# Kernel tuning notes

Measured on AMD Instinct MI355X. Metric: run time of the kernel, lower is better.

Reference implementation:

```python
import jax, jax.numpy as jnp
import numpy as np

N_GROUPS = 8
TOPK_GROUPS = 4
TOPK = 8
ROUTE_SCALE = 2.5

def setup_inputs() -> dict:
    key = jax.random.key(0)
    k1, k2, k3 = jax.random.split(key, 3)
    B, D, E = 8192, 7168, 256
    x = jax.random.normal(k1, (B, D), dtype=jnp.float32)
    weight = jax.random.normal(k2, (E, D), dtype=jnp.float32) / np.sqrt(D)
    bias = jax.random.normal(k3, (E,), dtype=jnp.float32) * 0.01
    return {"x": x, "weight": weight, "bias": bias}

def reference(x, weight, bias):
    B = x.shape[0]
    # linear scores: (B, E)
    scores = jnp.einsum('bd,ed->be', x, weight)
    # sigmoid score function
    s = jax.nn.sigmoid(scores)
    original_scores = s
    # bias correction for group selection (bias is not None since dim==7168)
    sb = s + bias
    # group view: (B, G, E/G)
    sg = sb.reshape(B, N_GROUPS, -1)
    # group score = sum of top-2 per group (bias branch)
    group_scores = jax.lax.top_k(sg, 2)[0].sum(axis=-1)  # (B, G)
    gidx = jax.lax.top_k(group_scores, TOPK_GROUPS)[1]   # (B, topk_groups)
    # boolean mask of selected groups
    gmask = jnp.zeros((B, N_GROUPS), dtype=bool).at[jnp.arange(B)[:, None], gidx].set(True)
    sg = jnp.where(gmask[:, :, None], sg, -jnp.inf)
    flat = sg.reshape(B, -1)  # (B, E)
    indices = jax.lax.top_k(flat, TOPK)[1]               # (B, topk)
    weights = jnp.take_along_axis(original_scores, indices, axis=1)
    # sigmoid path: normalize to sum 1, then scale
    weights = weights / weights.sum(axis=-1, keepdims=True)
    weights = weights * ROUTE_SCALE
    return weights.astype(x.dtype), indices
```

## Files before the change

### kernel.cpp

```cpp
#include <hip/hip_runtime.h>
#include <hip/hip_bf16.h>
#include <math.h>

#define DDIM 7168
#define NEXP 256
#define NGRP 8
#define TOPKG 4
#define TOPK 8
#define ROUTE_SCALE 2.5f

#define BM 64
#define BN 256
#define BK 32
#define KSPLIT 4
#define KPER (DDIM / KSPLIT)
#define NSTEP (KPER / BK)
#define NKTILE (DDIM / BK)
#define BT_ELEMS (NEXP * BK * 2)

typedef __attribute__((ext_vector_type(8))) short bf16x8;
typedef __attribute__((ext_vector_type(4))) float f32x4;
typedef unsigned int u32;
typedef unsigned short ushort_t;

static __device__ __forceinline__ ushort_t bf16_rne(float f) {
    u32 b = __float_as_uint(f);
    u32 r = (b + 0x7fffu + ((b >> 16) & 1u)) >> 16;
    return (ushort_t)r;
}
static __device__ __forceinline__ float bf16_to_f32(ushort_t h) {
    return __uint_as_float(((u32)h) << 16);
}
static __device__ __forceinline__ void split_elem(float f, short& h, short& l) {
    union { __hip_bfloat16 b; short s; } cv;
    cv.b = __float2bfloat16(f);
    h = cv.s;
    float hf = __uint_as_float(((u32)(ushort_t)cv.s) << 16);
    cv.b = __float2bfloat16(f - hf);
    l = cv.s;
}

__global__ __launch_bounds__(256) void wsplit_kernel(const float* __restrict__ w,
                                                     short* __restrict__ wsp)
{
    const int kt = blockIdx.x;
    const int e  = threadIdx.x;
    const float* wp = w + (size_t)e * DDIM + (size_t)kt * BK;
    short* tb = wsp + (size_t)kt * BT_ELEMS;
    const int fn = e >> 4, er = e & 15;
    #pragma unroll
    for (int jg = 0; jg < 4; jg++) {
        float f[8];
        *(float4*)&f[0] = *(const float4*)(wp + jg * 8);
        *(float4*)&f[4] = *(const float4*)(wp + jg * 8 + 4);
        ushort_t h[8], l[8];
        #pragma unroll
        for (int j = 0; j < 8; j++) {
            h[j] = bf16_rne(f[j]);
            l[j] = bf16_rne(f[j] - bf16_to_f32(h[j]));
        }
        const int lane = jg * 16 + er;
        *(uint4*)(tb + ((size_t)(0 * 16 + fn) * 64 + lane) * 8) = *(uint4*)h;
        *(uint4*)(tb + ((size_t)(1 * 16 + fn) * 64 + lane) * 8) = *(uint4*)l;
    }
}

__global__ __launch_bounds__(512, 2) void gemm_split_kernel(
    const float* __restrict__ x, const short* __restrict__ wsp,
    float* __restrict__ part, int Btok)
{
    __shared__ short Blds[2][BT_ELEMS];
    __shared__ float Alds[2][BM * BK];

    const int bid  = blockIdx.x;
    const int xcd  = bid & 7;
    const int ksp  = xcd & 3;
    const int mt   = (bid >> 3) * 2 + (xcd >> 2);
    const int m0   = mt * BM;
    const int kbase = ksp * KPER;
    const int t    = threadIdx.x;
    const int wid  = t >> 6, lane = t & 63;
    const int wm   = wid >> 2, wn = wid & 3;
    const int lr   = lane & 15, lg = lane >> 4;

    const short* wt0 = wsp + (size_t)(ksp * NSTEP) * BT_ELEMS;

    const int arow  = wid * 8 + (lane >> 3);
    const int akoff = 4 * ((lane & 7) ^ ((lane >> 3) & 7));
    const float* asrc0 = x + (size_t)(m0 + arow) * DDIM + kbase + akoff;
    const int adst_off = wid * 1024 + lane * 16;

#define STAGE_B(stp, buf) do {                                                             \
        const short* gt_ = wt0 + (size_t)(stp) * BT_ELEMS;                                 \
        _Pragma("unroll")                                                                  \
        for (int i_ = 0; i_ < 4; i_++) {                                                   \
            const int off_ = wid * 4096 + i_ * 1024;                                       \
            __builtin_amdgcn_global_load_lds(                                              \
                (const __attribute__((address_space(1))) u32*)((const char*)gt_ + off_ + lane * 16), \
                (__attribute__((address_space(3))) u32*)((char*)&Blds[buf][0] + off_),     \
                16, 0, 0);                                                                 \
        } } while (0)

#define STAGE_A(stp, buf) do {                                                             \
        __builtin_amdgcn_global_load_lds(                                                  \
            (const __attribute__((address_space(1))) u32*)(asrc0 + (size_t)(stp) * BK),    \
            (__attribute__((address_space(3))) u32*)((char*)&Alds[buf][0] + adst_off),     \
            16, 0, 0);                                                                     \
    } while (0)

    f32x4 acc[2][4];
    #pragma unroll
    for (int i = 0; i < 2; i++)
        #pragma unroll
        for (int j = 0; j < 4; j++) acc[i][j] = (f32x4){0.f, 0.f, 0.f, 0.f};

    STAGE_B(0, 0);
    STAGE_A(0, 0);

    for (int st = 0; st < NSTEP; st++) {
        const int cur = st & 1;
        __syncthreads();

        if (st + 1 < NSTEP) {
            STAGE_B(st + 1, cur ^ 1);
            STAGE_A(st + 1, cur ^ 1);
        }

        const char* ab = (const char*)&Alds[cur][0];
        bf16x8 ah[2], al[2];
        #pragma unroll
        for (int fm = 0; fm < 2; fm++) {
            const int row = wm * 32 + fm * 16 + lr;
            const int rb  = row * 128;
            const int sw  = (lr & 7) << 4;
            float fr[8];
            *(float4*)&fr[0] = *(const float4*)(ab + rb + ((lg * 32) ^ sw));
            *(float4*)&fr[4] = *(const float4*)(ab + rb + ((lg * 32 + 16) ^ sw));
            union { bf16x8 v; short s[8]; } H, L;
            #pragma unroll
            for (int j = 0; j < 8; j++)
                split_elem(fr[j], H.s[j], L.s[j]);
            ah[fm] = H.v;
            al[fm] = L.v;
        }

        bf16x8 bhv[4], blv[4];
        #pragma unroll
        for (int fn = 0; fn < 4; fn++) {
            bhv[fn] = *(const bf16x8*)&Blds[cur][((size_t)(0 * 16 + wn * 4 + fn) * 64 + lane) * 8];
            blv[fn] = *(const bf16x8*)&Blds[cur][((size_t)(1 * 16 + wn * 4 + fn) * 64 + lane) * 8];
        }
        #pragma unroll
        for (int fn = 0; fn < 4; fn++)
            #pragma unroll
            for (int fm = 0; fm < 2; fm++)
                acc[fm][fn] = __builtin_amdgcn_mfma_f32_16x16x32_bf16(ah[fm], bhv[fn], acc[fm][fn], 0, 0, 0);
        #pragma unroll
        for (int fn = 0; fn < 4; fn++)
            #pragma unroll
            for (int fm = 0; fm < 2; fm++)
                acc[fm][fn] = __builtin_amdgcn_mfma_f32_16x16x32_bf16(ah[fm], blv[fn], acc[fm][fn], 0, 0, 0);
        #pragma unroll
        for (int fn = 0; fn < 4; fn++)
            #pragma unroll
            for (int fm = 0; fm < 2; fm++)
                acc[fm][fn] = __builtin_amdgcn_mfma_f32_16x16x32_bf16(al[fm], bhv[fn], acc[fm][fn], 0, 0, 0);
    }
#undef STAGE_B
#undef STAGE_A

    float* pp = part + (size_t)ksp * (size_t)Btok * NEXP;
    #pragma unroll
    for (int fm = 0; fm < 2; fm++) {
        const int row0 = m0 + wm * 32 + fm * 16 + lg * 4;
        #pragma unroll
        for (int fn = 0; fn < 4; fn++) {
            const int col = wn * 64 + fn * 16 + lr;
            #pragma unroll
            for (int rr = 0; rr < 4; rr++)
                pp[(size_t)(row0 + rr) * NEXP + col] = acc[fm][fn][rr];
        }
    }
}

__global__ __launch_bounds__(256) void gate_kernel(
    const float* __restrict__ part, const float* __restrict__ bias,
    float* __restrict__ out_w, float* __restrict__ out_i, int B)
{
    const int lane = threadIdx.x & 63;
    const int wid  = threadIdx.x >> 6;
    const int row  = blockIdx.x * 4 + wid;
    if (row >= B) return;

    const size_t plane = (size_t)B * NEXP;
    const float* pr = part + (size_t)row * NEXP + lane * 4;
    float4 v0 = *(const float4*)(pr);
    float4 v1 = *(const float4*)(pr + plane);
    float4 v2 = *(const float4*)(pr + 2 * plane);
    float4 v3 = *(const float4*)(pr + 3 * plane);
    float sc[4] = { v0.x + v1.x + v2.x + v3.x,
                    v0.y + v1.y + v2.y + v3.y,
                    v0.z + v1.z + v2.z + v3.z,
                    v0.w + v1.w + v2.w + v3.w };
    float4 bv = *(const float4*)(bias + lane * 4);
    const float bb[4] = { bv.x, bv.y, bv.z, bv.w };

    float so[4], sb[4];
    #pragma unroll
    for (int j = 0; j < 4; j++) {
        so[j] = 1.0f / (1.0f + expf(-sc[j]));
        sb[j] = so[j] + bb[j];
    }

    float m1 = sb[0], m2 = -INFINITY;
    #pragma unroll
    for (int j = 1; j < 4; j++) {
        if (sb[j] > m1)      { m2 = m1; m1 = sb[j]; }
        else if (sb[j] > m2) { m2 = sb[j]; }
    }
    #pragma unroll
    for (int m = 1; m <= 4; m <<= 1) {
        float o1 = __shfl_xor(m1, m);
        float o2 = __shfl_xor(m2, m);
        float hi = fmaxf(m1, o1);
        float lo = fminf(m1, o1);
        m1 = hi;
        m2 = fmaxf(lo, fmaxf(m2, o2));
    }
    float gscore = m1 + m2;
    int g = lane >> 3;

    float gs[NGRP];
    #pragma unroll
    for (int gg = 0; gg < NGRP; gg++) gs[gg] = __shfl(gscore, gg * 8);
    int rank = 0;
    #pragma unroll
    for (int gg = 0; gg < NGRP; gg++) {
        if (gg == g) continue;
        if (gs[gg] > gs[g] || (gs[gg] == gs[g] && gg < g)) rank++;
    }
    const bool selg = (rank < TOPKG);
    float mv[4];
    #pragma unroll
    for (int j = 0; j < 4; j++) mv[j] = selg ? sb[j] : -INFINITY;

    float wsel[TOPK];
    int   isel[TOPK];
    float wsum = 0.f;
    #pragma unroll
    for (int it = 0; it < TOPK; it++) {
        float v = mv[0]; int jj = 0;
        #pragma unroll
        for (int j = 1; j < 4; j++)
            if (mv[j] > v) { v = mv[j]; jj = j; }
        int gi = (lane << 2) | jj;
        #pragma unroll
        for (int m = 1; m < 64; m <<= 1) {
            float ov = __shfl_xor(v, m);
            int   oi = __shfl_xor(gi, m);
            if (ov > v || (ov == v && oi < gi)) { v = ov; gi = oi; }
        }
        int slot = gi & 3, src = gi >> 2;
        float cand = (slot == 0) ? so[0] : (slot == 1) ? so[1] : (slot == 2) ? so[2] : so[3];
        float sval = __shfl(cand, src);
        wsel[it] = sval; isel[it] = gi; wsum += sval;
        if (lane == src) mv[slot] = -INFINITY;
    }

    if (lane == 0) {
        float scl = ROUTE_SCALE / wsum;
        #pragma unroll
        for (int it = 0; it < TOPK; it++) {
            out_w[(size_t)row * TOPK + it] = wsel[it] * scl;
            out_i[(size_t)row * TOPK + it] = (float)isel[it];
        }
    }
}

extern "C" void kernel_launch(void* const* d_in, const int* in_sizes, int n_in,
                              void* d_out, int out_size, void* d_ws, size_t ws_size,
                              hipStream_t stream)
{
    const float* x    = (const float*)d_in[0];
    const float* w    = (const float*)d_in[1];
    const float* bias = (const float*)d_in[2];
    const int B = in_sizes[0] / DDIM;

    float* part = (float*)d_ws;
    short* wsp  = (short*)((char*)d_ws + (size_t)KSPLIT * B * NEXP * sizeof(float));

    float* out_w = (float*)d_out;
    float* out_i = out_w + (size_t)B * TOPK;

    hipLaunchKernelGGL(wsplit_kernel, dim3(NKTILE), dim3(256), 0, stream, w, wsp);
    hipLaunchKernelGGL(gemm_split_kernel, dim3((B / BM) * KSPLIT), dim3(512), 0, stream,
                       x, wsp, part, B);
    hipLaunchKernelGGL(gate_kernel, dim3((B + 3) / 4), dim3(256), 0, stream,
                       part, bias, out_w, out_i, B);
}
```

Before: 126.3 us.

## Double the M tile to 128 and triple-buffer LDS staging with explicit waitcnts

Doubles the per-block M tile so each staged weight tile (hi/lo bf16 split) feeds four 16-row fragments instead of two. This halves how often the weight slab is re-read per token row. The LDS pipeline goes from double to triple buffering with rotating pointers and manual s_waitcnt vmcnt/lgkmcnt plus a raw barrier, so two stages are in flight at once. In exchange, LDS use and accumulator registers roughly double, which may cut occupancy below the declared two blocks per CU. The manual wait counts must also exactly match the loads issued per stage.

```diff
diff --git a/kernel.cpp b/kernel.cpp
--- a/kernel.cpp
+++ b/kernel.cpp
@@ -9,7 +9,7 @@
 #define TOPK 8
 #define ROUTE_SCALE 2.5f
 
-#define BM 64
+#define BM 128
 #define BN 256
 #define BK 32
 #define KSPLIT 4
@@ -17,6 +17,7 @@
 #define NSTEP (KPER / BK)
 #define NKTILE (DDIM / BK)
 #define BT_ELEMS (NEXP * BK * 2)
+#define AT_FLOATS (BM * BK)
 
 typedef __attribute__((ext_vector_type(8))) short bf16x8;
 typedef __attribute__((ext_vector_type(4))) float f32x4;
@@ -69,8 +70,8 @@
     const float* __restrict__ x, const short* __restrict__ wsp,
     float* __restrict__ part, int Btok)
 {
-    __shared__ short Blds[2][BT_ELEMS];
-    __shared__ float Alds[2][BM * BK];
+    __shared__ short Blds[3][BT_ELEMS];
+    __shared__ float Alds[3][AT_FLOATS];
 
     const int bid  = blockIdx.x;
     const int xcd  = bid & 7;
@@ -85,52 +86,58 @@
 
     const short* wt0 = wsp + (size_t)(ksp * NSTEP) * BT_ELEMS;
 
-    const int arow  = wid * 8 + (lane >> 3);
+    const int arow0 = wid * 16 + (lane >> 3);
     const int akoff = 4 * ((lane & 7) ^ ((lane >> 3) & 7));
-    const float* asrc0 = x + (size_t)(m0 + arow) * DDIM + kbase + akoff;
-    const int adst_off = wid * 1024 + lane * 16;
-
-#define STAGE_B(stp, buf) do {                                                             \
+    const float* asrc0 = x + (size_t)(m0 + arow0) * DDIM + kbase + akoff;
+    const size_t arow_step = (size_t)8 * DDIM;
+    const int adst0 = wid * 2048 + lane * 16;
+
+#define STAGE_B(stp, bptr) do {                                                            \
         const short* gt_ = wt0 + (size_t)(stp) * BT_ELEMS;                                 \
         _Pragma("unroll")                                                                  \
         for (int i_ = 0; i_ < 4; i_++) {                                                   \
             const int off_ = wid * 4096 + i_ * 1024;                                       \
             __builtin_amdgcn_global_load_lds(                                              \
                 (const __attribute__((address_space(1))) u32*)((const char*)gt_ + off_ + lane * 16), \
-                (__attribute__((address_space(3))) u32*)((char*)&Blds[buf][0] + off_),     \
+                (__attribute__((address_space(3))) u32*)((char*)(bptr) + off_),            \
                 16, 0, 0);                                                                 \
         } } while (0)
 
-#define STAGE_A(stp, buf) do {                                                             \
-        __builtin_amdgcn_global_load_lds(                                                  \
-            (const __attribute__((address_space(1))) u32*)(asrc0 + (size_t)(stp) * BK),    \
-            (__attribute__((address_space(3))) u32*)((char*)&Alds[buf][0] + adst_off),     \
-            16, 0, 0);                                                                     \
-    } while (0)
-
-    f32x4 acc[2][4];
-    #pragma unroll
-    for (int i = 0; i < 2; i++)
+#define STAGE_A(stp, aptr) do {                                                            \
+        _Pragma("unroll")                                                                  \
+        for (int i_ = 0; i_ < 2; i_++) {                                                   \
+            __builtin_amdgcn_global_load_lds(                                              \
+                (const __attribute__((address_space(1))) u32*)(asrc0 + (size_t)i_ * arow_step + (size_t)(stp) * BK), \
+                (__attribute__((address_space(3))) u32*)((char*)(aptr) + adst0 + i_ * 1024), \
+                16, 0, 0);                                                                 \
+        } } while (0)
+
+    f32x4 acc[4][4];
+    #pragma unroll
+    for (int i = 0; i < 4; i++)
         #pragma unroll
         for (int j = 0; j < 4; j++) acc[i][j] = (f32x4){0.f, 0.f, 0.f, 0.f};
 
-    STAGE_B(0, 0);
-    STAGE_A(0, 0);
+    short* pB_r = &Blds[0][0]; short* pB_1 = &Blds[1][0]; short* pB_2 = &Blds[2][0];
+    float* pA_r = &Alds[0][0]; float* pA_1 = &Alds[1][0]; float* pA_2 = &Alds[2][0];
+
+    STAGE_B(0, pB_r); STAGE_A(0, pA_r);
+    STAGE_B(1, pB_1); STAGE_A(1, pA_1);
 
     for (int st = 0; st < NSTEP; st++) {
-        const int cur = st & 1;
-        __syncthreads();
-
-        if (st + 1 < NSTEP) {
-            STAGE_B(st + 1, cur ^ 1);
-            STAGE_A(st + 1, cur ^ 1);
-        }
-
-        const char* ab = (const char*)&Alds[cur][0];
-        bf16x8 ah[2], al[2];
-        #pragma unroll
-        for (int fm = 0; fm < 2; fm++) {
-            const int row = wm * 32 + fm * 16 + lr;
+        if (st < NSTEP - 1) { asm volatile("s_waitcnt vmcnt(6)" ::: "memory"); }
+        else                { asm volatile("s_waitcnt vmcnt(0)" ::: "memory"); }
+        asm volatile("s_waitcnt lgkmcnt(0)" ::: "memory");
+        __builtin_amdgcn_s_barrier();
+        asm volatile("" ::: "memory");
+
+        if (st + 2 < NSTEP) { STAGE_B(st + 2, pB_2); STAGE_A(st + 2, pA_2); }
+
+        const char* ab = (const char*)pA_r;
+        bf16x8 ah[4], al[4];
+        #pragma unroll
+        for (int fm = 0; fm < 4; fm++) {
+            const int row = wm * 64 + fm * 16 + lr;
             const int rb  = row * 128;
             const int sw  = (lr & 7) << 4;
             float fr[8];
@@ -147,32 +154,35 @@
         bf16x8 bhv[4], blv[4];
         #pragma unroll
         for (int fn = 0; fn < 4; fn++) {
-            bhv[fn] = *(const bf16x8*)&Blds[cur][((size_t)(0 * 16 + wn * 4 + fn) * 64 + lane) * 8];
-            blv[fn] = *(const bf16x8*)&Blds[cur][((size_t)(1 * 16 + wn * 4 + fn) * 64 + lane) * 8];
+            bhv[fn] = *(const bf16x8*)&pB_r[((size_t)(0 * 16 + wn * 4 + fn) * 64 + lane) * 8];
+            blv[fn] = *(const bf16x8*)&pB_r[((size_t)(1 * 16 + wn * 4 + fn) * 64 + lane) * 8];
         }
         #pragma unroll
         for (int fn = 0; fn < 4; fn++)
             #pragma unroll
-            for (int fm = 0; fm < 2; fm++)
+            for (int fm = 0; fm < 4; fm++)
                 acc[fm][fn] = __builtin_amdgcn_mfma_f32_16x16x32_bf16(ah[fm], bhv[fn], acc[fm][fn], 0, 0, 0);
         #pragma unroll
         for (int fn = 0; fn < 4; fn++)
             #pragma unroll
-            for (int fm = 0; fm < 2; fm++)
+            for (int fm = 0; fm < 4; fm++)
                 acc[fm][fn] = __builtin_amdgcn_mfma_f32_16x16x32_bf16(ah[fm], blv[fn], acc[fm][fn], 0, 0, 0);
         #pragma unroll
         for (int fn = 0; fn < 4; fn++)
             #pragma unroll
-            for (int fm = 0; fm < 2; fm++)
+            for (int fm = 0; fm < 4; fm++)
                 acc[fm][fn] = __builtin_amdgcn_mfma_f32_16x16x32_bf16(al[fm], bhv[fn], acc[fm][fn], 0, 0, 0);
+
+        { short* tb_ = pB_r; pB_r = pB_1; pB_1 = pB_2; pB_2 = tb_; }
+        { float* ta_ = pA_r; pA_r = pA_1; pA_1 = pA_2; pA_2 = ta_; }
     }
 #undef STAGE_B
 #undef STAGE_A
 
     float* pp = part + (size_t)ksp * (size_t)Btok * NEXP;
     #pragma unroll
-    for (int fm = 0; fm < 2; fm++) {
-        const int row0 = m0 + wm * 32 + fm * 16 + lg * 4;
+    for (int fm = 0; fm < 4; fm++) {
+        const int row0 = m0 + wm * 64 + fm * 16 + lg * 4;
         #pragma unroll
         for (int fn = 0; fn < 4; fn++) {
             const int col = wn * 64 + fn * 16 + lr;
```

New measurement: 144.3 us. 14.3% more time.

## Triple-buffer LDS, stage only hi weights, read lo weights from global

Applied to the files above, without the earlier changes.

The GEMM moves from a double-buffered to a triple-buffered LDS pipeline that prefetches two steps ahead and waits with vmcnt(3) instead of a full __syncthreads. Only the high bf16 half of the split weights is staged into LDS; the low half is loaded directly from global into registers. This cuts LDS use per block so launch bounds can request 4 blocks per CU instead of 2. The trade-off is extra per-wave global traffic for the low weights, higher register pressure, and a fragile hand-tuned waitcnt scheme.

```diff
diff --git a/kernel.cpp b/kernel.cpp
--- a/kernel.cpp
+++ b/kernel.cpp
@@ -17,6 +17,8 @@
 #define NSTEP (KPER / BK)
 #define NKTILE (DDIM / BK)
 #define BT_ELEMS (NEXP * BK * 2)
+#define BH_ELEMS (NEXP * BK)
+#define AT_FLOATS (BM * BK)
 
 typedef __attribute__((ext_vector_type(8))) short bf16x8;
 typedef __attribute__((ext_vector_type(4))) float f32x4;
@@ -65,12 +67,12 @@
     }
 }
 
-__global__ __launch_bounds__(512, 2) void gemm_split_kernel(
+__global__ __launch_bounds__(512, 4) void gemm_split_kernel(
     const float* __restrict__ x, const short* __restrict__ wsp,
     float* __restrict__ part, int Btok)
 {
-    __shared__ short Blds[2][BT_ELEMS];
-    __shared__ float Alds[2][BM * BK];
+    __shared__ short Blds[3][BH_ELEMS];
+    __shared__ float Alds[3][AT_FLOATS];
 
     const int bid  = blockIdx.x;
     const int xcd  = bid & 7;
@@ -90,21 +92,19 @@
     const float* asrc0 = x + (size_t)(m0 + arow) * DDIM + kbase + akoff;
     const int adst_off = wid * 1024 + lane * 16;
 
-#define STAGE_B(stp, buf) do {                                                             \
+#define STAGE_GRP(stp, bptr, aptr) do {                                                    \
         const short* gt_ = wt0 + (size_t)(stp) * BT_ELEMS;                                 \
         _Pragma("unroll")                                                                  \
-        for (int i_ = 0; i_ < 4; i_++) {                                                   \
-            const int off_ = wid * 4096 + i_ * 1024;                                       \
+        for (int i_ = 0; i_ < 2; i_++) {                                                   \
+            const int off_ = wid * 2048 + i_ * 1024;                                       \
             __builtin_amdgcn_global_load_lds(                                              \
                 (const __attribute__((address_space(1))) u32*)((const char*)gt_ + off_ + lane * 16), \
-                (__attribute__((address_space(3))) u32*)((char*)&Blds[buf][0] + off_),     \
+                (__attribute__((address_space(3))) u32*)((char*)(bptr) + off_),            \
                 16, 0, 0);                                                                 \
-        } } while (0)
-
-#define STAGE_A(stp, buf) do {                                                             \
+        }                                                                                  \
         __builtin_amdgcn_global_load_lds(                                                  \
             (const __attribute__((address_space(1))) u32*)(asrc0 + (size_t)(stp) * BK),    \
-            (__attribute__((address_space(3))) u32*)((char*)&Alds[buf][0] + adst_off),     \
+            (__attribute__((address_space(3))) u32*)((char*)(aptr) + adst_off),            \
             16, 0, 0);                                                                     \
     } while (0)
 
@@ -114,19 +114,27 @@
         #pragma unroll
         for (int j = 0; j < 4; j++) acc[i][j] = (f32x4){0.f, 0.f, 0.f, 0.f};
 
-    STAGE_B(0, 0);
-    STAGE_A(0, 0);
+    short* pB_r = &Blds[0][0]; short* pB_1 = &Blds[1][0]; short* pB_2 = &Blds[2][0];
+    float* pA_r = &Alds[0][0]; float* pA_1 = &Alds[1][0]; float* pA_2 = &Alds[2][0];
+
+    STAGE_GRP(0, pB_r, pA_r);
+    STAGE_GRP(1, pB_1, pA_1);
 
     for (int st = 0; st < NSTEP; st++) {
-        const int cur = st & 1;
-        __syncthreads();
-
-        if (st + 1 < NSTEP) {
-            STAGE_B(st + 1, cur ^ 1);
-            STAGE_A(st + 1, cur ^ 1);
-        }
-
-        const char* ab = (const char*)&Alds[cur][0];
+        asm volatile("s_waitcnt vmcnt(3)" ::: "memory");
+        asm volatile("s_waitcnt lgkmcnt(0)" ::: "memory");
+        __builtin_amdgcn_s_barrier();
+
+        const short* blo = wt0 + (size_t)st * BT_ELEMS + BH_ELEMS;
+        bf16x8 blv[4];
+        #pragma unroll
+        for (int fn = 0; fn < 4; fn++)
+            blv[fn] = *(const bf16x8*)&blo[((size_t)(wn * 4 + fn) * 64 + lane) * 8];
+        __builtin_amdgcn_sched_barrier(0);
+
+        if (st + 2 < NSTEP) STAGE_GRP(st + 2, pB_2, pA_2);
+
+        const char* ab = (const char*)pA_r;
         bf16x8 ah[2], al[2];
         #pragma unroll
         for (int fm = 0; fm < 2; fm++) {
@@ -144,12 +152,11 @@
             al[fm] = L.v;
         }
 
-        bf16x8 bhv[4], blv[4];
-        #pragma unroll
-        for (int fn = 0; fn < 4; fn++) {
-            bhv[fn] = *(const bf16x8*)&Blds[cur][((size_t)(0 * 16 + wn * 4 + fn) * 64 + lane) * 8];
-            blv[fn] = *(const bf16x8*)&Blds[cur][((size_t)(1 * 16 + wn * 4 + fn) * 64 + lane) * 8];
-        }
+        bf16x8 bhv[4];
+        #pragma unroll
+        for (int fn = 0; fn < 4; fn++)
+            bhv[fn] = *(const bf16x8*)&pB_r[((size_t)(wn * 4 + fn) * 64 + lane) * 8];
+
         #pragma unroll
         for (int fn = 0; fn < 4; fn++)
             #pragma unroll
@@ -159,15 +166,17 @@
         for (int fn = 0; fn < 4; fn++)
             #pragma unroll
             for (int fm = 0; fm < 2; fm++)
+                acc[fm][fn] = __builtin_amdgcn_mfma_f32_16x16x32_bf16(al[fm], bhv[fn], acc[fm][fn], 0, 0, 0);
+        #pragma unroll
+        for (int fn = 0; fn < 4; fn++)
+            #pragma unroll
+            for (int fm = 0; fm < 2; fm++)
                 acc[fm][fn] = __builtin_amdgcn_mfma_f32_16x16x32_bf16(ah[fm], blv[fn], acc[fm][fn], 0, 0, 0);
-        #pragma unroll
-        for (int fn = 0; fn < 4; fn++)
-            #pragma unroll
-            for (int fm = 0; fm < 2; fm++)
-                acc[fm][fn] = __builtin_amdgcn_mfma_f32_16x16x32_bf16(al[fm], bhv[fn], acc[fm][fn], 0, 0, 0);
-    }
-#undef STAGE_B
-#undef STAGE_A
+
+        { short* tb_ = pB_r; pB_r = pB_1; pB_1 = pB_2; pB_2 = tb_; }
+        { float* ta_ = pA_r; pA_r = pA_1; pA_1 = pA_2; pA_2 = ta_; }
+    }
+#undef STAGE_GRP
 
     float* pp = part + (size_t)ksp * (size_t)Btok * NEXP;
     #pragma unroll
```

Result: slower. 146.4 us (+16.0%).
